# Performance work log

Hardware: AMD Instinct MI355X
Metric: run time of the kernel (lower is better)

## Reference

```python
import jax, jax.numpy as jnp
from jax import lax
import numpy as np
import math

D = 256  # pyramid feature_size

def _conv(x, w, b, stride, pad):
    y = lax.conv_general_dilated(x, w, (stride, stride), [(pad, pad), (pad, pad)],
                                 dimension_numbers=('NCHW', 'OIHW', 'NCHW'))
    return y + b[None, :, None, None]

def _pe(L, d=D):
    pos = np.arange(L, dtype=np.float32)[:, None]
    div = np.exp(np.arange(0, d, 2, dtype=np.float32) * (-math.log(10000.0) / float(d)))
    pe = np.zeros((L, d), np.float32)
    pe[:, 0::2] = np.sin(pos * div)
    pe[:, 1::2] = np.cos(pos * div)
    return jnp.asarray(pe)

def _up_nearest(x, H, W):
    hi = jnp.arange(H) * x.shape[2] // H
    wi = jnp.arange(W) * x.shape[3] // W
    return x[:, :, hi][:, :, :, wi]

def setup_inputs() -> dict:
    key = jax.random.key(0)
    ks = jax.random.split(key, 24)
    rn = lambda k, s, std=1.0: jax.random.normal(k, s, jnp.float32) * std
    B, S = 8, 5
    z = lambda: jnp.zeros((D,), jnp.float32)
    return {
        'C3': rn(ks[0], (B, 512, 40, 40)),
        'C4': rn(ks[1], (B, 1024, 20, 20)),
        'C5': rn(ks[2], (B, 2048, 10, 10)),
        'S3': rn(ks[3], (B * S, 512, 40, 40)),
        'S4': rn(ks[4], (B * S, 1024, 20, 20)),
        'S5': rn(ks[5], (B * S, 2048, 10, 10)),
        'p3_1_w': rn(ks[6], (D, 512, 1, 1), 0.02), 'p3_1_b': z(),
        'p3_2_w': rn(ks[7], (D, D, 3, 3), 0.02), 'p3_2_b': z(),
        'p4_1_w': rn(ks[8], (D, 1024, 1, 1), 0.02), 'p4_1_b': z(),
        'p4_2_w': rn(ks[9], (D, D, 3, 3), 0.02), 'p4_2_b': z(),
        'p5_1_w': rn(ks[10], (D, 2048, 1, 1), 0.02), 'p5_1_b': z(),
        'p5_2_w': rn(ks[11], (D, D, 3, 3), 0.02), 'p5_2_b': z(),
        'p6_w': rn(ks[12], (D, 2048, 3, 3), 0.02), 'p6_b': z(),
        'p7_w': rn(ks[13], (D, D, 3, 3), 0.02), 'p7_b': z(),
        'q_w': rn(ks[14], (D, D), 0.01), 'q_b': z(),
        'k_w': rn(ks[15], (D, D), 0.01), 'k_b': z(),
    }

def reference(C3, C4, C5, S3, S4, S5,
              p3_1_w, p3_1_b, p3_2_w, p3_2_b,
              p4_1_w, p4_1_b, p4_2_w, p4_2_b,
              p5_1_w, p5_1_b, p5_2_w, p5_2_b,
              p6_w, p6_b, p7_w, p7_b, q_w, q_b, k_w, k_b):
    B = C3.shape[0]
    S = S3.shape[0] // B
    # FPN lateral 1x1 convs (query and support share weights)
    P5x = _conv(C5, p5_1_w, p5_1_b, 1, 0)
    P4x = _conv(C4, p4_1_w, p4_1_b, 1, 0)
    P3x = _conv(C3, p3_1_w, p3_1_b, 1, 0)
    P5s = _conv(S5, p5_1_w, p5_1_b, 1, 0)
    P4s = _conv(S4, p4_1_w, p4_1_b, 1, 0)
    P3s = _conv(S3, p3_1_w, p3_1_b, 1, 0)
    P6x = _conv(C5, p6_w, p6_b, 2, 1)
    P7x = _conv(jax.nn.relu(P6x), p7_w, p7_b, 2, 1)
    P6s = _conv(S5, p6_w, p6_b, 2, 1)
    P7s = _conv(jax.nn.relu(P6s), p7_w, p7_b, 2, 1)
    # top-down pathway (order matches torch source)
    P5u = _up_nearest(P5x, P4x.shape[2], P4x.shape[3])
    P5x = _conv(P5x, p5_2_w, p5_2_b, 1, 1)
    P4x = P5u + P4x
    P4u = _up_nearest(P4x, P3x.shape[2], P3x.shape[3])
    P4x = _conv(P4x, p4_2_w, p4_2_b, 1, 1)
    P3x = _conv(P3x + P4u, p3_2_w, p3_2_b, 1, 1)

    def to_shots(t):  # [B*S,C,H,W] -> [S,B,C,H,W]
        return t.reshape(B, S, t.shape[1], t.shape[2], t.shape[3]).transpose(1, 0, 2, 3, 4)

    qs = [P3x, P4x, P5x, P6x, P7x]
    ss = [to_shots(P3s), to_shots(P4s), to_shots(P5s), to_shots(P6s), to_shots(P7s)]
    outs = []
    scale = math.sqrt(float(D))
    for qx, sx in zip(qs, ss):
        H, W = qx.shape[2], qx.shape[3]
        q = qx.reshape(B, D, H * W).transpose(0, 2, 1)           # [B, HW, D]
        Q = q @ q_w.T + q_b
        L = sx.shape[3] * sx.shape[4]
        s = sx.reshape(S, B, D, L).transpose(0, 1, 3, 2) + _pe(L)  # [S, B, L, D]
        K = s @ k_w.T + k_b
        att = jax.nn.softmax(jnp.einsum('bqd,sbkd->sbqk', Q, K) / scale, axis=-1)
        m = jnp.einsum('sbqk,sbkd->bqd', att, s) / S              # mean over shots fused
        outs.append(jnp.concatenate([qx, m.transpose(0, 2, 1).reshape(B, D, H, W)], axis=1))
    return tuple(outs)
```

## Files before the change

### kernel.cpp

```cpp
#include <hip/hip_runtime.h>
#include <hip/hip_bf16.h>
#include <math.h>

#define LK 72

typedef __hip_bfloat16 bf16;
typedef __bf16 bf16x8 __attribute__((ext_vector_type(8)));
typedef __bf16 bf16x4v __attribute__((ext_vector_type(4)));
typedef float  f32x4  __attribute__((ext_vector_type(4)));

__global__ __launch_bounds__(256)
void pe_init_kernel(float* __restrict__ peT) {
    const int d = blockIdx.x;
    const int j = d >> 1;
    const double dv = exp(-(double)(2 * j) * 9.210340371976184 / 256.0);
    for (int l = threadIdx.x; l < 1600; l += 256) {
        const float arg = (float)l * (float)dv;
        peT[(size_t)d * 1600 + l] = (d & 1) ? cosf(arg) : sinf(arg);
    }
}

__global__ void repack_w(const float* __restrict__ w, __bf16* __restrict__ dst,
                         int Cin, int ksq)
{
    const int total = 256 * Cin * ksq;
    const int idx = blockIdx.x * 256 + threadIdx.x;
    if (idx >= total) return;
    const int o = idx / (Cin * ksq);
    const int r = idx - o * Cin * ksq;
    const int c = r / ksq;
    const int sh = r - c * ksq;
    dst[((size_t)sh * 256 + o) * Cin + c] = (__bf16)w[idx];
}

__global__ void addpe_kernel(const bf16* __restrict__ s, const float* __restrict__ peT,
                             bf16* __restrict__ spe, int L, int total)
{
    const int idx = blockIdx.x * 256 + threadIdx.x;
    if (idx >= total) return;
    const int l = idx % L;
    const int c = (idx / L) & 255;
    spe[idx] = __float2bfloat16(__bfloat162float(s[idx]) + peT[(size_t)c * 1600 + l]);
}

__global__ void bias_init_kernel(float* __restrict__ out, const float* __restrict__ bias,
                                 int N, int total)
{
    const int idx = blockIdx.x * 256 + threadIdx.x;
    if (idx >= total) return;
    out[idx] = bias[(idx / N) & 255];
}

__global__ void cast_f32_bf16(const float* __restrict__ src, bf16* __restrict__ dst,
                              int total)
{
    const int idx = blockIdx.x * 256 + threadIdx.x;
    if (idx < total) dst[idx] = __float2bfloat16(src[idx]);
}

__global__ __launch_bounds__(256)
void gemm1x1_mfma(const void* __restrict__ in, const __bf16* __restrict__ wbf,
                  const float* __restrict__ bias, void* __restrict__ out,
                  int Cin, int N, int in_bf16, int out_mode)
{
    const int b  = blockIdx.z;
    const int o0 = blockIdx.y * 64;
    const int n0 = blockIdx.x * 64;
    const int t  = threadIdx.x;
    const int wv  = t >> 6;
    const int ln  = t & 63;
    const int lm  = ln & 15;
    const int kq8 = (ln >> 4) * 8;

    __shared__ __bf16 Bs[64][LK];

    f32x4 acc[4];
    #pragma unroll
    for (int ct = 0; ct < 4; ++ct) acc[ct] = (f32x4){0.f, 0.f, 0.f, 0.f};

    const int cg = t >> 4;
    const int ng = t & 15;
    const int nb = n0 + ng * 4;
    const bool vec_ok = ((N & 3) == 0) && (nb + 3 < N);

    const float*  inf = (const float*)in;
    const __bf16* inh = (const __bf16*)in;
    const size_t inb0 = (size_t)b * Cin * N;

    const __bf16* arow = wbf + (size_t)(o0 + wv * 16 + lm) * Cin;

    for (int c0 = 0; c0 < Cin; c0 += 64) {
        __syncthreads();
        float rv[4][4];
        #pragma unroll
        for (int i = 0; i < 4; ++i) {
            const int c = c0 + cg * 4 + i;
            const size_t base = inb0 + (size_t)c * N + nb;
            if (vec_ok) {
                if (in_bf16) {
                    const bf16x4v v = *(const bf16x4v*)&inh[base];
                    rv[i][0] = (float)v[0]; rv[i][1] = (float)v[1];
                    rv[i][2] = (float)v[2]; rv[i][3] = (float)v[3];
                } else {
                    const float4 v = *(const float4*)&inf[base];
                    rv[i][0] = v.x; rv[i][1] = v.y; rv[i][2] = v.z; rv[i][3] = v.w;
                }
            } else {
                #pragma unroll
                for (int jj = 0; jj < 4; ++jj) {
                    const int n = nb + jj;
                    rv[i][jj] = (n < N) ? (in_bf16 ? (float)inh[inb0 + (size_t)c * N + n]
                                                   : inf[inb0 + (size_t)c * N + n])
                                        : 0.f;
                }
            }
        }
        #pragma unroll
        for (int jj = 0; jj < 4; ++jj) {
            bf16x4v pk;
            pk[0] = (__bf16)rv[0][jj]; pk[1] = (__bf16)rv[1][jj];
            pk[2] = (__bf16)rv[2][jj]; pk[3] = (__bf16)rv[3][jj];
            *(bf16x4v*)&Bs[ng * 4 + jj][cg * 4] = pk;
        }
        __syncthreads();

        #pragma unroll
        for (int k0 = 0; k0 < 64; k0 += 32) {
            const bf16x8 a = *(const bf16x8*)&arow[c0 + k0 + kq8];
            #pragma unroll
            for (int ct = 0; ct < 4; ++ct) {
                const bf16x8 bb = *(const bf16x8*)&Bs[ct * 16 + lm][k0 + kq8];
                acc[ct] = __builtin_amdgcn_mfma_f32_16x16x32_bf16(a, bb, acc[ct], 0, 0, 0);
            }
        }
    }

    const int rbase = o0 + wv * 16 + (ln >> 4) * 4;
    #pragma unroll
    for (int ct = 0; ct < 4; ++ct) {
        const int col = n0 + ct * 16 + lm;
        if (col < N) {
            if (out_mode == 2) {
                bf16x4v pk;
                #pragma unroll
                for (int r = 0; r < 4; ++r)
                    pk[r] = (__bf16)(acc[ct][r] + bias[rbase + r]);
                *(bf16x4v*)&((__bf16*)out)[((size_t)b * N + col) * 256 + rbase] = pk;
            } else {
                const size_t outb = (size_t)b * 256 * N;
                #pragma unroll
                for (int r = 0; r < 4; ++r) {
                    const int o = rbase + r;
                    const float val = acc[ct][r] + bias[o];
                    if (out_mode == 1) ((__bf16*)out)[outb + (size_t)o * N + col] = (__bf16)val;
                    else               ((float*)out)[outb + (size_t)o * N + col] = val;
                }
            }
        }
    }
}

__global__ __launch_bounds__(256)
void conv3x3h_mfma(const void* __restrict__ in, const __bf16* __restrict__ wbf,
                   const float* __restrict__ bias, void* __restrict__ out,
                   const float* __restrict__ addup,
                   int Cin, int H, int W, int in_bf16, int out_bf16)
{
    const int b  = blockIdx.z;
    const int o0 = blockIdx.y * 64;
    const int n0 = blockIdx.x * 64;
    const int N  = H * W;
    const int EXT = 64 + 2 * W + 2;
    const int t  = threadIdx.x;
    const int wv = t >> 6;
    const int ln = t & 63;
    const int lm = ln & 15;
    const int kq8 = (ln >> 4) * 8;

    __shared__ __bf16 Bs[146][LK];

    f32x4 acc[4];
    #pragma unroll
    for (int ct = 0; ct < 4; ++ct) acc[ct] = (f32x4){0.f, 0.f, 0.f, 0.f};

    const size_t inb0 = (size_t)b * Cin * N;
    const int upH = H >> 1, upW = W >> 1;
    const float* addb = addup ? addup + (size_t)b * Cin * upH * upW : nullptr;
    const float*  inf = (const float*)in;
    const __bf16* inh = (const __bf16*)in;

    int yct[4], xct[4];
    bool nok[4];
    #pragma unroll
    for (int ct = 0; ct < 4; ++ct) {
        const int n = n0 + ct * 16 + lm;
        nok[ct] = n < N;
        yct[ct] = nok[ct] ? n / W : 0;
        xct[ct] = nok[ct] ? n - yct[ct] * W : 0;
    }

    bf16x8 zro;
    #pragma unroll
    for (int j = 0; j < 8; ++j) zro[j] = (__bf16)0.f;

    const int srow = t & 63;
    const int kb16 = (t >> 6) * 16;
    const int basep = n0 - W - 1;

    for (int c0 = 0; c0 < Cin; c0 += 64) {
        __syncthreads();
        for (int rb = 0; rb < EXT; rb += 64) {
            const int row = rb + srow;
            if (row < EXT) {
                const int p = basep + row;
                const bool ok = (p >= 0) && (p < N);
                const int py = ok ? p / W : 0;
                const int px = ok ? p - py * W : 0;
                #pragma unroll
                for (int j = 0; j < 16; ++j) {
                    const int kk = kb16 + j;
                    const int c  = c0 + kk;
                    float v = 0.f;
                    if (ok) {
                        v = in_bf16 ? (float)inh[inb0 + (size_t)c * N + p]
                                    : inf[inb0 + (size_t)c * N + p];
                        if (addb) v += addb[((size_t)c * upH + (py >> 1)) * upW + (px >> 1)];
                    }
                    Bs[row][kk] = (__bf16)v;
                }
            }
        }
        __syncthreads();

        #pragma unroll
        for (int sh = 0; sh < 9; ++sh) {
            const int ky = sh / 3, kx = sh - ky * 3;
            const int off = (ky - 1) * W + (kx - 1) + W + 1;
            bool vm[4];
            #pragma unroll
            for (int ct = 0; ct < 4; ++ct)
                vm[ct] = nok[ct] && (unsigned)(yct[ct] + ky - 1) < (unsigned)H
                                 && (unsigned)(xct[ct] + kx - 1) < (unsigned)W;
            const __bf16* ash = wbf + ((size_t)sh * 256 + o0 + wv * 16 + lm) * Cin + c0;
            #pragma unroll
            for (int k0 = 0; k0 < 64; k0 += 32) {
                const bf16x8 a = *(const bf16x8*)&ash[k0 + kq8];
                #pragma unroll
                for (int ct = 0; ct < 4; ++ct) {
                    bf16x8 bb = *(const bf16x8*)&Bs[ct * 16 + lm + off][k0 + kq8];
                    bb = vm[ct] ? bb : zro;
                    acc[ct] = __builtin_amdgcn_mfma_f32_16x16x32_bf16(a, bb, acc[ct], 0, 0, 0);
                }
            }
        }
    }

    const size_t outb = (size_t)b * 256 * N;
    const int rbase = o0 + wv * 16 + (ln >> 4) * 4;
    #pragma unroll
    for (int ct = 0; ct < 4; ++ct) {
        const int col = n0 + ct * 16 + lm;
        if (col < N) {
            #pragma unroll
            for (int r = 0; r < 4; ++r) {
                const int o = rbase + r;
                const float val = acc[ct][r] + bias[o];
                if (out_bf16) ((__bf16*)out)[outb + (size_t)o * N + col] = (__bf16)val;
                else          ((float*)out)[outb + (size_t)o * N + col] = val;
            }
        }
    }
}

__global__ __launch_bounds__(256)
void convsk_mfma(const void* __restrict__ in, const __bf16* __restrict__ wbf,
                 float* __restrict__ out,
                 int B, int Cin, int Hin, int Win, int Ho, int Wo,
                 int ks, int stride, int pad, int relu_in, int in_bf16,
                 int kchunk)
{
    const int N  = Ho * Wo;
    const int NT = B * N;
    const int col0 = blockIdx.x * 64;
    const int t  = threadIdx.x;
    const int wv = t >> 6;
    const int ln = t & 63;
    const int lm = ln & 15;
    const int kq8 = (ln >> 4) * 8;

    __shared__ __bf16 Bs[64][LK];

    f32x4 acc[4][4];
    #pragma unroll
    for (int rt = 0; rt < 4; ++rt)
        #pragma unroll
        for (int ct = 0; ct < 4; ++ct) acc[rt][ct] = (f32x4){0.f, 0.f, 0.f, 0.f};

    const size_t inHW = (size_t)Hin * Win;
    const int ksq = ks * ks;
    const float*  inf = (const float*)in;
    const __bf16* inh = (const __bf16*)in;

    const int srow = t & 63;
    const int kb16 = (t >> 6) * 16;
    const int scol = col0 + srow;
    const bool cvalid = scol < NT;
    int sb = 0, yo = 0, xo = 0;
    if (cvalid) {
        sb = scol / N;
        const int sn = scol - sb * N;
        yo = sn / Wo; xo = sn - yo * Wo;
    }

    const int Ktot = Cin * ksq;
    const int kbeg = blockIdx.y * kchunk;
    const int kend = min(kbeg + kchunk, Ktot);

    for (int k0 = kbeg; k0 < kend; k0 += 64) {
        const int sh = k0 / Cin;
        const int c0 = k0 - sh * Cin;
        const int ky = sh / ks, kx = sh - ky * ks;
        const int iy = yo * stride + ky - pad;
        const int ix = xo * stride + kx - pad;
        const bool ld_ok = cvalid && iy >= 0 && iy < Hin && ix >= 0 && ix < Win;
        const size_t sidx = (size_t)sb * Cin * inHW + (size_t)iy * Win + ix;

        __syncthreads();
        #pragma unroll
        for (int j = 0; j < 16; ++j) {
            const int kk = kb16 + j;
            const int c  = c0 + kk;
            float v = 0.f;
            if (ld_ok) {
                v = in_bf16 ? (float)inh[sidx + (size_t)c * inHW]
                            : inf[sidx + (size_t)c * inHW];
                if (relu_in) v = fmaxf(v, 0.f);
            }
            Bs[srow][kk] = (__bf16)v;
        }
        __syncthreads();

        #pragma unroll
        for (int k32 = 0; k32 < 64; k32 += 32) {
            bf16x8 bfr[4];
            #pragma unroll
            for (int ct = 0; ct < 4; ++ct)
                bfr[ct] = *(const bf16x8*)&Bs[ct * 16 + lm][k32 + kq8];
            #pragma unroll
            for (int rt = 0; rt < 4; ++rt) {
                const __bf16* ap = wbf + ((size_t)sh * 256 + wv * 64 + rt * 16 + lm) * Cin
                                       + c0 + k32 + kq8;
                const bf16x8 a = *(const bf16x8*)ap;
                #pragma unroll
                for (int ct = 0; ct < 4; ++ct)
                    acc[rt][ct] = __builtin_amdgcn_mfma_f32_16x16x32_bf16(a, bfr[ct],
                                                                          acc[rt][ct], 0, 0, 0);
            }
        }
    }

    const int rb0 = wv * 64 + (ln >> 4) * 4;
    #pragma unroll
    for (int ct = 0; ct < 4; ++ct) {
        const int col = col0 + ct * 16 + lm;
        if (col < NT) {
            const int be = col / N;
            const int ne = col - be * N;
            float* ob = out + (size_t)be * 256 * N + ne;
            #pragma unroll
            for (int rt = 0; rt < 4; ++rt)
                #pragma unroll
                for (int r = 0; r < 4; ++r)
                    atomicAdd(&ob[(size_t)(rb0 + rt * 16 + r) * N], acc[rt][ct][r]);
        }
    }
}

__global__ void add_up_kernel(const float* __restrict__ a, const float* __restrict__ up,
                              float* __restrict__ o, int H, int W, int total)
{
    const int idx = blockIdx.x * 256 + threadIdx.x;
    if (idx >= total) return;
    const int x = idx % W;
    const int tmp = idx / W;
    const int y = tmp % H;
    const int bc = tmp / H;
    o[idx] = a[idx] + up[((size_t)bc * (H >> 1) + (y >> 1)) * (W >> 1) + (x >> 1)];
}

__global__ __launch_bounds__(256)
void attn_mfma(const __bf16* __restrict__ Qrow, const __bf16* __restrict__ Krow,
               const bf16* __restrict__ Sv, float* __restrict__ outp, int L, int S)
{
    const int b  = blockIdx.y;
    const int s  = blockIdx.z;
    const int q0 = blockIdx.x * 64;
    const int t  = threadIdx.x;
    const int wv = t >> 6;
    const int ln = t & 63;
    const int lm = ln & 15;
    const int lg = ln >> 4;

    __shared__ __bf16 Ks[32][264];
    __shared__ __bf16 Vt[256][40];
    __shared__ __bf16 Pl[4][16][40];

    bf16x8 qf[8];
    {
        const int q = q0 + wv * 16 + lm;
        if (q < L) {
            const __bf16* qp = Qrow + ((size_t)b * L + q) * 256 + lg * 8;
            #pragma unroll
            for (int sl = 0; sl < 8; ++sl) qf[sl] = *(const bf16x8*)&qp[sl * 32];
        } else {
            #pragma unroll
            for (int sl = 0; sl < 8; ++sl)
                #pragma unroll
                for (int j = 0; j < 8; ++j) qf[sl][j] = (__bf16)0.f;
        }
    }

    f32x4 acc[16];
    #pragma unroll
    for (int ds = 0; ds < 16; ++ds) acc[ds] = (f32x4){0.f, 0.f, 0.f, 0.f};
    float m_run[4] = {-INFINITY, -INFINITY, -INFINITY, -INFINITY};
    float l_run[4] = {0.f, 0.f, 0.f, 0.f};

    const size_t kbase = (size_t)(b * S + s) * L * 256;
    const __bf16* vb0  = (const __bf16*)Sv + (size_t)(b * S + s) * 256 * L;

    const int nt = (L + 31) >> 5;
    for (int lt = 0; lt < nt; ++lt) {
        const int l0 = lt << 5;
        __syncthreads();
        {
            const int row = t >> 3, cb = (t & 7) * 32;
            const int l = l0 + row;
            if (l < L) {
                const __bf16* src = Krow + kbase + (size_t)l * 256 + cb;
                #pragma unroll
                for (int j = 0; j < 4; ++j)
                    *(bf16x8*)&Ks[row][cb + j * 8] = *(const bf16x8*)&src[j * 8];
            } else {
                #pragma unroll
                for (int j = 0; j < 32; ++j) Ks[row][cb + j] = (__bf16)0.f;
            }
        }
        {
            const __bf16* src = vb0 + (size_t)t * L + l0;
            if (l0 + 32 <= L && ((((size_t)src) & 15) == 0)) {
                #pragma unroll
                for (int j = 0; j < 4; ++j)
                    *(bf16x8*)&Vt[t][j * 8] = *(const bf16x8*)&src[j * 8];
            } else {
                #pragma unroll
                for (int j = 0; j < 32; ++j)
                    Vt[t][j] = (l0 + j < L) ? src[j] : (__bf16)0.f;
            }
        }
        __syncthreads();

        f32x4 sc0 = (f32x4){0.f, 0.f, 0.f, 0.f};
        f32x4 sc1 = (f32x4){0.f, 0.f, 0.f, 0.f};
        #pragma unroll
        for (int sl = 0; sl < 8; ++sl) {
            const bf16x8 k0 = *(const bf16x8*)&Ks[lm][sl * 32 + lg * 8];
            const bf16x8 k1 = *(const bf16x8*)&Ks[16 + lm][sl * 32 + lg * 8];
            sc0 = __builtin_amdgcn_mfma_f32_16x16x32_bf16(qf[sl], k0, sc0, 0, 0, 0);
            sc1 = __builtin_amdgcn_mfma_f32_16x16x32_bf16(qf[sl], k1, sc1, 0, 0, 0);
        }

        const bool v0 = (l0 + lm) < L;
        const bool v1 = (l0 + 16 + lm) < L;
        float p0[4], p1[4], mt[4];
        #pragma unroll
        for (int r = 0; r < 4; ++r) {
            const float a = v0 ? sc0[r] * 0.0625f : -INFINITY;
            const float c = v1 ? sc1[r] * 0.0625f : -INFINITY;
            p0[r] = a; p1[r] = c; mt[r] = fmaxf(a, c);
        }
        #pragma unroll
        for (int w = 1; w < 16; w <<= 1)
            #pragma unroll
            for (int r = 0; r < 4; ++r) mt[r] = fmaxf(mt[r], __shfl_xor(mt[r], w, 16));
        float alpha[4], rs[4];
        #pragma unroll
        for (int r = 0; r < 4; ++r) {
            const float mn = fmaxf(m_run[r], mt[r]);
            alpha[r] = __expf(m_run[r] - mn);
            p0[r] = v0 ? __expf(p0[r] - mn) : 0.f;
            p1[r] = v1 ? __expf(p1[r] - mn) : 0.f;
            m_run[r] = mn;
            rs[r] = p0[r] + p1[r];
        }
        #pragma unroll
        for (int w = 1; w < 16; w <<= 1)
            #pragma unroll
            for (int r = 0; r < 4; ++r) rs[r] += __shfl_xor(rs[r], w, 16);
        #pragma unroll
        for (int r = 0; r < 4; ++r) l_run[r] = l_run[r] * alpha[r] + rs[r];
        #pragma unroll
        for (int ds = 0; ds < 16; ++ds)
            #pragma unroll
            for (int r = 0; r < 4; ++r) acc[ds][r] *= alpha[r];

        #pragma unroll
        for (int r = 0; r < 4; ++r) {
            Pl[wv][lg * 4 + r][lm]      = (__bf16)p0[r];
            Pl[wv][lg * 4 + r][16 + lm] = (__bf16)p1[r];
        }
        const bf16x8 pa = *(const bf16x8*)&Pl[wv][lm][lg * 8];

        #pragma unroll
        for (int ds = 0; ds < 16; ++ds) {
            const bf16x8 vv = *(const bf16x8*)&Vt[ds * 16 + lm][lg * 8];
            acc[ds] = __builtin_amdgcn_mfma_f32_16x16x32_bf16(pa, vv, acc[ds], 0, 0, 0);
        }
    }

    const int qrow = q0 + wv * 16 + lg * 4;
    float inv[4];
    #pragma unroll
    for (int r = 0; r < 4; ++r) inv[r] = 1.f / (l_run[r] * (float)S);
    #pragma unroll
    for (int ds = 0; ds < 16; ++ds) {
        const int d = ds * 16 + lm;
        float* ob = outp + ((size_t)b * 512 + 256 + d) * L;
        #pragma unroll
        for (int r = 0; r < 4; ++r) {
            const int q = qrow + r;
            if (q < L) atomicAdd(&ob[q], acc[ds][r] * inv[r]);
        }
    }
}

__global__ void zero_attn_half(float* __restrict__ outp, int L, int total)
{
    const int idx = blockIdx.x * 256 + threadIdx.x;
    if (idx >= total) return;
    const int b = idx / (256 * L);
    const int r = idx - b * 256 * L;
    outp[((size_t)b * 512 + 256) * L + r] = 0.f;
}

__global__ void copy_cast_kernel(const void* __restrict__ src, float* __restrict__ dst,
                                 int HW, int total, int in_bf16)
{
    const int idx = blockIdx.x * 256 + threadIdx.x;
    if (idx >= total) return;
    const int b = idx / (256 * HW);
    const int r = idx - b * 256 * HW;
    const float v = in_bf16 ? __bfloat162float(((const bf16*)src)[idx])
                            : ((const float*)src)[idx];
    dst[(size_t)b * 512 * HW + r] = v;
}

extern "C" void kernel_launch(void* const* d_in, const int* in_sizes, int n_in,
                              void* d_out, int out_size, void* d_ws, size_t ws_size,
                              hipStream_t stream)
{
    (void)in_sizes; (void)n_in; (void)out_size; (void)ws_size;
    const float* C3 = (const float*)d_in[0];
    const float* C4 = (const float*)d_in[1];
    const float* C5 = (const float*)d_in[2];
    const float* S3 = (const float*)d_in[3];
    const float* S4 = (const float*)d_in[4];
    const float* S5 = (const float*)d_in[5];
    const float* p31w = (const float*)d_in[6];  const float* p31b = (const float*)d_in[7];
    const float* p32w = (const float*)d_in[8];  const float* p32b = (const float*)d_in[9];
    const float* p41w = (const float*)d_in[10]; const float* p41b = (const float*)d_in[11];
    const float* p42w = (const float*)d_in[12]; const float* p42b = (const float*)d_in[13];
    const float* p51w = (const float*)d_in[14]; const float* p51b = (const float*)d_in[15];
    const float* p52w = (const float*)d_in[16]; const float* p52b = (const float*)d_in[17];
    const float* p6w  = (const float*)d_in[18]; const float* p6b  = (const float*)d_in[19];
    const float* p7w  = (const float*)d_in[20]; const float* p7b  = (const float*)d_in[21];
    const float* qw   = (const float*)d_in[22]; const float* qb   = (const float*)d_in[23];
    const float* kw   = (const float*)d_in[24]; const float* kb   = (const float*)d_in[25];
    float* out = (float*)d_out;

    uint8_t* base = (uint8_t*)d_ws;
    size_t off = 0;
    auto A = [&](size_t bytes) { size_t r = off; off += (bytes + 255) & ~(size_t)255; return r; };
    float* pPE  = (float*)(base + A((size_t)256 * 1600 * 4));
    bf16*  pP3q = (bf16*) (base + A((size_t)8  * 256 * 1600 * 2));
    float* pP4q = (float*)(base + A((size_t)8  * 256 * 400  * 4));
    float* pP5q = (float*)(base + A((size_t)8  * 256 * 100  * 4));
    bf16*  pP3s = (bf16*) (base + A((size_t)40 * 256 * 1600 * 2));
    bf16*  pP4s = (bf16*) (base + A((size_t)40 * 256 * 400  * 2));
    bf16*  pP5s = (bf16*) (base + A((size_t)40 * 256 * 100  * 2));
    float* pP6q = (float*)(base + A((size_t)8  * 256 * 25   * 4));
    float* pP7q = (float*)(base + A((size_t)8  * 256 * 9    * 4));
    float* pP6sF= (float*)(base + A((size_t)40 * 256 * 25   * 4));
    float* pP7sF= (float*)(base + A((size_t)40 * 256 * 9    * 4));
    bf16*  pP6s = (bf16*) (base + A((size_t)40 * 256 * 25   * 2));
    bf16*  pP7s = (bf16*) (base + A((size_t)40 * 256 * 9    * 2));
    float* pP4m = (float*)(base + A((size_t)8  * 256 * 400  * 4));
    float* pP5f = (float*)(base + A((size_t)8  * 256 * 100  * 4));
    float* pP4f = (float*)(base + A((size_t)8  * 256 * 400  * 4));
    bf16*  pP3f = (bf16*) (base + A((size_t)8  * 256 * 1600 * 2));
    __bf16* pQ  = (__bf16*)(base + A((size_t)8  * 1600 * 256 * 2));
    __bf16* pK  = (__bf16*)(base + A((size_t)40 * 1600 * 256 * 2));
    bf16*  pSPE = (bf16*) (base + A((size_t)40 * 256 * 1600 * 2));
    __bf16* r31 = (__bf16*)(base + A((size_t)256 * 512 * 2));
    __bf16* r32 = (__bf16*)(base + A((size_t)256 * 256 * 9 * 2));
    __bf16* r41 = (__bf16*)(base + A((size_t)256 * 1024 * 2));
    __bf16* r42 = (__bf16*)(base + A((size_t)256 * 256 * 9 * 2));
    __bf16* r51 = (__bf16*)(base + A((size_t)256 * 2048 * 2));
    __bf16* r52 = (__bf16*)(base + A((size_t)256 * 256 * 9 * 2));
    __bf16* r6  = (__bf16*)(base + A((size_t)256 * 2048 * 9 * 2));
    __bf16* r7  = (__bf16*)(base + A((size_t)256 * 256 * 9 * 2));
    __bf16* rq  = (__bf16*)(base + A((size_t)256 * 256 * 2));
    __bf16* rk  = (__bf16*)(base + A((size_t)256 * 256 * 2));

    pe_init_kernel<<<dim3(256), dim3(256), 0, stream>>>(pPE);

    auto rep = [&](const float* w, __bf16* dst, int Cin, int ksq) {
        const int total = 256 * Cin * ksq;
        repack_w<<<dim3((total + 255) / 256), dim3(256), 0, stream>>>(w, dst, Cin, ksq);
    };
    rep(p31w, r31, 512, 1);  rep(p32w, r32, 256, 9);
    rep(p41w, r41, 1024, 1); rep(p42w, r42, 256, 9);
    rep(p51w, r51, 2048, 1); rep(p52w, r52, 256, 9);
    rep(p6w,  r6,  2048, 9); rep(p7w,  r7,  256, 9);
    rep(qw,   rq,  256, 1);  rep(kw,   rk,  256, 1);

    auto g1 = [&](const void* in, const __bf16* wbf, const float* bias, void* o,
                  int B, int Cin, int N, int in_bf16, int out_mode) {
        dim3 g((N + 63) / 64, 4, B);
        gemm1x1_mfma<<<g, dim3(256), 0, stream>>>(in, wbf, bias, o, Cin, N,
                                                  in_bf16, out_mode);
    };
    auto ch3 = [&](const void* in, const __bf16* wbf, const float* bias, void* o,
                   int B, int Cin, int H, int W, const float* addup,
                   int in_bf16, int out_bf16) {
        const int N = H * W;
        dim3 g((N + 63) / 64, 4, B);
        conv3x3h_mfma<<<g, dim3(256), 0, stream>>>(in, wbf, bias, o, addup,
                                                   Cin, H, W, in_bf16, out_bf16);
    };
    auto csk = [&](const void* in, const __bf16* wbf, const float* bias, float* o,
                   int B, int Cin, int Hin, int Win, int Ho, int Wo,
                   int stride, int pad, int relu_in, int in_bf16, int kchunk) {
        const int N = Ho * Wo;
        const int NT = B * N;
        const int Ktot = Cin * 9;
        const int total = B * 256 * N;
        bias_init_kernel<<<dim3((total + 255) / 256), dim3(256), 0, stream>>>(
            o, bias, N, total);
        dim3 g((NT + 63) / 64, (Ktot + kchunk - 1) / kchunk, 1);
        convsk_mfma<<<g, dim3(256), 0, stream>>>(in, wbf, o, B, Cin, Hin, Win, Ho, Wo,
                                                 3, stride, pad, relu_in, in_bf16, kchunk);
    };

    g1(C3, r31, p31b, pP3q, 8,  512,  1600, 0, 1);
    g1(C4, r41, p41b, pP4q, 8,  1024, 400,  0, 0);
    g1(C5, r51, p51b, pP5q, 8,  2048, 100,  0, 0);
    g1(S3, r31, p31b, pP3s, 40, 512,  1600, 0, 1);
    g1(S4, r41, p41b, pP4s, 40, 1024, 400,  0, 1);
    g1(S5, r51, p51b, pP5s, 40, 2048, 100,  0, 1);
    csk(C5,    r6, p6b, pP6q,  8,  2048, 10, 10, 5, 5, 2, 1, 0, 0, 576);
    csk(S5,    r6, p6b, pP6sF, 40, 2048, 10, 10, 5, 5, 2, 1, 0, 0, 1152);
    {
        const int t6 = 40 * 256 * 25;
        cast_f32_bf16<<<dim3((t6 + 255) / 256), dim3(256), 0, stream>>>(pP6sF, pP6s, t6);
    }
    csk(pP6q,  r7, p7b, pP7q,  8,  256, 5, 5, 3, 3, 2, 1, 1, 0, 576);
    csk(pP6sF, r7, p7b, pP7sF, 40, 256, 5, 5, 3, 3, 2, 1, 1, 0, 576);
    {
        const int t7 = 40 * 256 * 9;
        cast_f32_bf16<<<dim3((t7 + 255) / 256), dim3(256), 0, stream>>>(pP7sF, pP7s, t7);
    }
    {
        const int total = 8 * 256 * 400;
        add_up_kernel<<<dim3((total + 255) / 256), dim3(256), 0, stream>>>(
            pP4q, pP5q, pP4m, 20, 20, total);
    }
    ch3(pP5q, r52, p52b, pP5f, 8, 256, 10, 10, nullptr, 0, 0);
    ch3(pP4m, r42, p42b, pP4f, 8, 256, 20, 20, nullptr, 0, 0);
    ch3(pP3q, r32, p32b, pP3f, 8, 256, 40, 40, pP4m, 1, 1);

    const int Ls[5] = {1600, 400, 100, 25, 9};
    const void* qsrc[5] = {pP3f, pP4f, pP5f, pP6q, pP7q};
    const int   qbf [5] = {1, 0, 0, 0, 0};
    const bf16* ssrc[5] = {pP3s, pP4s, pP5s, pP6s, pP7s};
    size_t ooff[5];
    {
        size_t ao = 0;
        for (int i = 0; i < 5; ++i) { ooff[i] = ao; ao += (size_t)8 * 512 * Ls[i]; }
    }
    for (int i = 0; i < 5; ++i) {
        const int L = Ls[i];
        const int stotal = 40 * 256 * L;
        addpe_kernel<<<dim3((stotal + 255) / 256), dim3(256), 0, stream>>>(
            ssrc[i], pPE, pSPE, L, stotal);
        g1(qsrc[i], rq, qb, pQ, 8, 256, L, qbf[i], 2);
        g1(pSPE, rk, kb, pK, 40, 256, L, 1, 2);
        const int total = 8 * 256 * L;
        zero_attn_half<<<dim3((total + 255) / 256), dim3(256), 0, stream>>>(
            out + ooff[i], L, total);
        attn_mfma<<<dim3((L + 63) / 64, 8, 5), dim3(256), 0, stream>>>(
            pQ, pK, pSPE, out + ooff[i], L, 5);
        copy_cast_kernel<<<dim3((total + 255) / 256), dim3(256), 0, stream>>>(
            qsrc[i], out + ooff[i], L, total, qbf[i]);
    }
}
```

Before: 2.052 ms.

## Prefetch K/V tiles into registers and skip softmax rescale when max unchanged

The attention kernel now loads the next K/V tile from global memory into registers while the current tile is computed, then writes it to shared memory at the start of the next iteration. This hides global-load latency behind MFMA work. Online-softmax rescaling of the 16 accumulators is skipped when no row max changes anywhere in the wave. The grid is also reordered so batch×shot is the fastest-varying block index. In exchange the kernel uses more registers (8 extra bf16x8 per thread), which may reduce occupancy.

```diff
diff --git a/kernel.cpp b/kernel.cpp
--- a/kernel.cpp
+++ b/kernel.cpp
@@ -392,9 +392,10 @@
 void attn_mfma(const __bf16* __restrict__ Qrow, const __bf16* __restrict__ Krow,
                const bf16* __restrict__ Sv, float* __restrict__ outp, int L, int S)
 {
-    const int b  = blockIdx.y;
-    const int s  = blockIdx.z;
-    const int q0 = blockIdx.x * 64;
+    const int bs = blockIdx.x;
+    const int b  = bs / 5;
+    const int s  = bs - b * 5;
+    const int q0 = blockIdx.y * 64;
     const int t  = threadIdx.x;
     const int wv = t >> 6;
     const int ln = t & 63;
@@ -429,36 +430,54 @@
     const size_t kbase = (size_t)(b * S + s) * L * 256;
     const __bf16* vb0  = (const __bf16*)Sv + (size_t)(b * S + s) * 256 * L;
 
+    const int krow_ = t >> 3;
+    const int kcb   = (t & 7) * 32;
+    const __bf16* vsrc0 = vb0 + (size_t)t * L;
+
+    bf16x8 kr[4], vr[4];
+    bf16x8 zro;
+    #pragma unroll
+    for (int j = 0; j < 8; ++j) zro[j] = (__bf16)0.f;
+
+    auto load_tile = [&](int l0) {
+        const int l = l0 + krow_;
+        if (l < L) {
+            const __bf16* src = Krow + kbase + (size_t)l * 256 + kcb;
+            #pragma unroll
+            for (int j = 0; j < 4; ++j) kr[j] = *(const bf16x8*)&src[j * 8];
+        } else {
+            #pragma unroll
+            for (int j = 0; j < 4; ++j) kr[j] = zro;
+        }
+        const __bf16* src = vsrc0 + l0;
+        if (l0 + 32 <= L && ((((size_t)src) & 15) == 0)) {
+            #pragma unroll
+            for (int j = 0; j < 4; ++j) vr[j] = *(const bf16x8*)&src[j * 8];
+        } else {
+            #pragma unroll
+            for (int j = 0; j < 4; ++j) {
+                #pragma unroll
+                for (int e = 0; e < 8; ++e) {
+                    const int l = l0 + j * 8 + e;
+                    vr[j][e] = (l < L) ? src[j * 8 + e] : (__bf16)0.f;
+                }
+            }
+        }
+    };
+
     const int nt = (L + 31) >> 5;
+    load_tile(0);
+
     for (int lt = 0; lt < nt; ++lt) {
+        __syncthreads();
+        #pragma unroll
+        for (int j = 0; j < 4; ++j) *(bf16x8*)&Ks[krow_][kcb + j * 8] = kr[j];
+        #pragma unroll
+        for (int j = 0; j < 4; ++j) *(bf16x8*)&Vt[t][j * 8] = vr[j];
+        if (lt + 1 < nt) load_tile((lt + 1) << 5);
+        __syncthreads();
+
         const int l0 = lt << 5;
-        __syncthreads();
-        {
-            const int row = t >> 3, cb = (t & 7) * 32;
-            const int l = l0 + row;
-            if (l < L) {
-                const __bf16* src = Krow + kbase + (size_t)l * 256 + cb;
-                #pragma unroll
-                for (int j = 0; j < 4; ++j)
-                    *(bf16x8*)&Ks[row][cb + j * 8] = *(const bf16x8*)&src[j * 8];
-            } else {
-                #pragma unroll
-                for (int j = 0; j < 32; ++j) Ks[row][cb + j] = (__bf16)0.f;
-            }
-        }
-        {
-            const __bf16* src = vb0 + (size_t)t * L + l0;
-            if (l0 + 32 <= L && ((((size_t)src) & 15) == 0)) {
-                #pragma unroll
-                for (int j = 0; j < 4; ++j)
-                    *(bf16x8*)&Vt[t][j * 8] = *(const bf16x8*)&src[j * 8];
-            } else {
-                #pragma unroll
-                for (int j = 0; j < 32; ++j)
-                    Vt[t][j] = (l0 + j < L) ? src[j] : (__bf16)0.f;
-            }
-        }
-        __syncthreads();
 
         f32x4 sc0 = (f32x4){0.f, 0.f, 0.f, 0.f};
         f32x4 sc1 = (f32x4){0.f, 0.f, 0.f, 0.f};
@@ -483,26 +502,41 @@
         for (int w = 1; w < 16; w <<= 1)
             #pragma unroll
             for (int r = 0; r < 4; ++r) mt[r] = fmaxf(mt[r], __shfl_xor(mt[r], w, 16));
-        float alpha[4], rs[4];
+
+        bool nochange = true;
+        #pragma unroll
+        for (int r = 0; r < 4; ++r) nochange = nochange && (mt[r] <= m_run[r]);
+        const bool skip = __all(nochange);
+
+        float mn[4], rs[4];
         #pragma unroll
         for (int r = 0; r < 4; ++r) {
-            const float mn = fmaxf(m_run[r], mt[r]);
-            alpha[r] = __expf(m_run[r] - mn);
-            p0[r] = v0 ? __expf(p0[r] - mn) : 0.f;
-            p1[r] = v1 ? __expf(p1[r] - mn) : 0.f;
-            m_run[r] = mn;
+            mn[r] = skip ? m_run[r] : fmaxf(m_run[r], mt[r]);
+            p0[r] = v0 ? __expf(p0[r] - mn[r]) : 0.f;
+            p1[r] = v1 ? __expf(p1[r] - mn[r]) : 0.f;
             rs[r] = p0[r] + p1[r];
         }
         #pragma unroll
         for (int w = 1; w < 16; w <<= 1)
             #pragma unroll
             for (int r = 0; r < 4; ++r) rs[r] += __shfl_xor(rs[r], w, 16);
-        #pragma unroll
-        for (int r = 0; r < 4; ++r) l_run[r] = l_run[r] * alpha[r] + rs[r];
-        #pragma unroll
-        for (int ds = 0; ds < 16; ++ds)
-            #pragma unroll
-            for (int r = 0; r < 4; ++r) acc[ds][r] *= alpha[r];
+
+        if (skip) {
+            #pragma unroll
+            for (int r = 0; r < 4; ++r) l_run[r] += rs[r];
+        } else {
+            float alpha[4];
+            #pragma unroll
+            for (int r = 0; r < 4; ++r) {
+                alpha[r] = __expf(m_run[r] - mn[r]);
+                l_run[r] = l_run[r] * alpha[r] + rs[r];
+                m_run[r] = mn[r];
+            }
+            #pragma unroll
+            for (int ds = 0; ds < 16; ++ds)
+                #pragma unroll
+                for (int r = 0; r < 4; ++r) acc[ds][r] *= alpha[r];
+        }
 
         #pragma unroll
         for (int r = 0; r < 4; ++r) {
@@ -698,7 +732,7 @@
         const int total = 8 * 256 * L;
         zero_attn_half<<<dim3((total + 255) / 256), dim3(256), 0, stream>>>(
             out + ooff[i], L, total);
-        attn_mfma<<<dim3((L + 63) / 64, 8, 5), dim3(256), 0, stream>>>(
+        attn_mfma<<<dim3(40, (L + 63) / 64), dim3(256), 0, stream>>>(
             pQ, pK, pSPE, out + ooff[i], L, 5);
         copy_cast_kernel<<<dim3((total + 255) / 256), dim3(256), 0, stream>>>(
             qsrc[i], out + ooff[i], L, total, qbf[i]);
```

After: 2.182 ms. +6.3%, slower.
